# Kernel tuning notes

Hardware: AMD Instinct MI355X
Metric: run time of the kernel (lower is better)

The kernel has to match this reference:

```python
import jax, jax.numpy as jnp
import numpy as np


def _maxpool2x2(t):
    # t: [B, C, H, W] -> [B, C, H//2, W//2]
    b, c, h, w = t.shape
    return t.reshape(b, c, h // 2, 2, w // 2, 2).max(axis=(3, 5))


def setup_inputs() -> dict:
    key = jax.random.key(0)
    ks = jax.random.split(key, 6)
    B, C, H, W = 16, 64, 64, 64
    x = jax.random.normal(ks[0], (B, C, H, W), dtype=jnp.float32)
    # 1x1 conv weights (no bias), stored as [out_ch, in_ch]
    s = 0.05
    W_theta = jax.random.normal(ks[1], (C // 8, C), dtype=jnp.float32) * s
    W_phi = jax.random.normal(ks[2], (C // 8, C), dtype=jnp.float32) * s
    W_g = jax.random.normal(ks[3], (C // 2, C), dtype=jnp.float32) * s
    W_attn = jax.random.normal(ks[4], (C, C // 2), dtype=jnp.float32) * s
    sigma = jnp.ones((1,), dtype=jnp.float32) * 0.5  # nonzero so attn path matters
    return {"x": x, "W_theta": W_theta, "W_phi": W_phi, "W_g": W_g,
            "W_attn": W_attn, "sigma": sigma}


def reference(x, W_theta, W_phi, W_g, W_attn, sigma):
    B, C, H, W = x.shape
    N = H * W
    M = N // 4
    # 1x1 convs are channel matmuls
    theta = jnp.einsum('oc,bchw->bohw', W_theta, x).reshape(B, C // 8, N)      # [B, C/8, N]
    phi = _maxpool2x2(jnp.einsum('oc,bchw->bohw', W_phi, x)).reshape(B, C // 8, M)  # [B, C/8, M]
    attn = jax.nn.softmax(jnp.einsum('bkn,bkm->bnm', theta, phi), axis=-1)    # [B, N, M]
    g = _maxpool2x2(jnp.einsum('oc,bchw->bohw', W_g, x)).reshape(B, C // 2, M)  # [B, C/2, M]
    attn_g = jnp.einsum('bgm,bnm->bgn', g, attn).reshape(B, C // 2, H, W)      # [B, C/2, H, W]
    attn_g = jnp.einsum('oc,bchw->bohw', W_attn, attn_g)                        # [B, C, H, W]
    return x + sigma * attn_g
```

## Files before the change

### kernel.cpp

```cpp
#include <hip/hip_runtime.h>
#include <hip/hip_bf16.h>

#define CC 64
#define NN 4096
#define MM 1024

typedef __attribute__((ext_vector_type(4))) short s4b;
typedef __attribute__((ext_vector_type(8))) short s8b;
typedef __attribute__((ext_vector_type(4))) float float4v;

__device__ inline unsigned short f2bf(float f) {
    union { float f; unsigned u; } v; v.f = f;
    unsigned r = v.u + 0x7fff + ((v.u >> 16) & 1);
    return (unsigned short)(r >> 16);
}

__device__ inline float4v mfma16(s4b a, s4b b, float4v c) {
#if __has_builtin(__builtin_amdgcn_mfma_f32_16x16x16bf16_1k)
    return __builtin_amdgcn_mfma_f32_16x16x16bf16_1k(a, b, c, 0, 0, 0);
#else
    float4v d;
    asm volatile("v_mfma_f32_16x16x16_bf16 %0, %1, %2, %3"
                 : "=v"(d) : "v"(a), "v"(b), "v"(c));
    return d;
#endif
}

__device__ inline float4v mfma32(s8b a, s8b b, float4v c) {
#if __has_builtin(__builtin_amdgcn_mfma_f32_16x16x32_bf16)
    return __builtin_amdgcn_mfma_f32_16x16x32_bf16(a, b, c, 0, 0, 0);
#else
    float4v d;
    asm volatile("v_mfma_f32_16x16x32_bf16 %0, %1, %2, %3"
                 : "=v"(d) : "v"(a), "v"(b), "v"(c));
    return d;
#endif
}

__global__ __launch_bounds__(256) void prep_kernel(
    const float* __restrict__ x,
    const float* __restrict__ Wth,
    const float* __restrict__ Wph,
    const float* __restrict__ Wg,
    unsigned short* __restrict__ thT,
    unsigned short* __restrict__ phiP,
    unsigned short* __restrict__ gP)
{
    constexpr int XP = 72;
    constexpr int DP = 49;

    __shared__ __align__(16) union {
        unsigned short xs[128 * XP];
        float bufD[128 * DP];
    } sh;

    const int tid  = threadIdx.x;
    const int b    = blockIdx.y;
    const int hp   = blockIdx.x;
    const int lane = tid & 63;
    const int wv   = tid >> 6;
    const int c15  = lane & 15;
    const int quad = lane >> 4;
    const int n0row = hp * 128;

    s8b wf[3][2];
    {
        const float* base0 = (c15 < 8) ? (Wth + c15 * 64)
                                       : (Wph + (c15 - 8) * 64);
        const float* base1 = Wg + c15 * 64;
        const float* base2 = Wg + (16 + c15) * 64;
        const float* bases[3] = {base0, base1, base2};
#pragma unroll
        for (int t = 0; t < 3; ++t) {
#pragma unroll
            for (int s = 0; s < 2; ++s) {
                const float* p = bases[t] + s * 32 + quad * 8;
                const float4 w0 = *(const float4*)p;
                const float4 w1 = *(const float4*)(p + 4);
                union { unsigned short us[8]; s8b v; } tmp;
                tmp.us[0] = f2bf(w0.x); tmp.us[1] = f2bf(w0.y);
                tmp.us[2] = f2bf(w0.z); tmp.us[3] = f2bf(w0.w);
                tmp.us[4] = f2bf(w1.x); tmp.us[5] = f2bf(w1.y);
                tmp.us[6] = f2bf(w1.z); tmp.us[7] = f2bf(w1.w);
                wf[t][s] = tmp.v;
            }
        }
    }

    {
        const int spx = tid & 127;
        const int chp = tid >> 7;
        const float* xb = x + (size_t)b * CC * NN + n0row + spx;
#pragma unroll
        for (int i = 0; i < 16; ++i) {
            const int c0 = i * 4 + chp * 2;
            const float va = xb[(size_t)c0 * NN];
            const float vb = xb[(size_t)(c0 + 1) * NN];
            const unsigned pk = (unsigned)f2bf(va) |
                                ((unsigned)f2bf(vb) << 16);
            *(unsigned*)&sh.xs[spx * XP + c0] = pk;
        }
    }
    __syncthreads();

    float4v acc[2][3];
#pragma unroll
    for (int tl = 0; tl < 2; ++tl)
#pragma unroll
        for (int t = 0; t < 3; ++t)
            acc[tl][t] = float4v{0.f, 0.f, 0.f, 0.f};

#pragma unroll
    for (int tl = 0; tl < 2; ++tl) {
        const int p0 = wv * 32 + tl * 16;
#pragma unroll
        for (int s = 0; s < 2; ++s) {
            union { uint4 u; s8b v; } bx;
            bx.u = *(const uint4*)&sh.xs[(p0 + c15) * XP + s * 32 + quad * 8];
#pragma unroll
            for (int t = 0; t < 3; ++t)
                acc[tl][t] = mfma32(wf[t][s], bx.v, acc[tl][t]);
        }
    }
    __syncthreads();

#pragma unroll
    for (int tl = 0; tl < 2; ++tl) {
        const int p0 = wv * 32 + tl * 16;
#pragma unroll
        for (int t = 0; t < 3; ++t)
#pragma unroll
            for (int r = 0; r < 4; ++r)
                sh.bufD[(p0 + c15) * DP + t * 16 + quad * 4 + r]
                    = acc[tl][t][r];
    }
    __syncthreads();

    if (tid < 128) {
        const int px = tid;
        union { unsigned short s_[8]; uint4 v; } pk;
#pragma unroll
        for (int j = 0; j < 8; ++j)
            pk.s_[j] = f2bf(sh.bufD[px * DP + j] * 1.44269504f);
        *(uint4*)&thT[((size_t)b * NN + n0row + px) * 8] = pk.v;
    }

    for (int idx = tid; idx < 1280; idx += 256) {
        const int pm = idx & 31;
        const int jj = idx >> 5;
        const int p00 = 2 * pm, p10 = 64 + 2 * pm;
        const float v = fmaxf(
            fmaxf(sh.bufD[p00 * DP + 8 + jj], sh.bufD[(p00 + 1) * DP + 8 + jj]),
            fmaxf(sh.bufD[p10 * DP + 8 + jj], sh.bufD[(p10 + 1) * DP + 8 + jj]));
        const int m = hp * 32 + pm;
        if (jj < 8) phiP[((size_t)b * MM + m) * 8 + jj] = f2bf(v);
        else        gP[((size_t)b * 32 + (jj - 8)) * MM + m] = f2bf(v);
    }
}

__global__ __launch_bounds__(256) void attn_mfma(
    const unsigned short* __restrict__ thT,
    const unsigned short* __restrict__ phiP,
    const unsigned short* __restrict__ gP,
    const float* __restrict__ x,
    const float* __restrict__ Wa,
    const float* __restrict__ sigma,
    float* __restrict__ out)
{
    constexpr int GP = 264;
    constexpr int OBP = 40;

    __shared__ __align__(16) union {
        struct {
            unsigned short phi[256 * 8 + 16];
            unsigned short g[32 * GP];
        } m;
        struct {
            float part[18][128];
            unsigned short obb[64 * OBP];
        } cb;
    } sh;

    const int tid  = threadIdx.x;
    const int lane = tid & 63;
    const int wv   = tid >> 6;
    const int wq   = wv & 1;
    const int wk   = wv >> 1;
    const int c15  = lane & 15;
    const int quad = lane >> 4;
    const int b    = blockIdx.y;
    const int n0   = blockIdx.x * 64;

    union { unsigned short s[8]; s8b v; } wfrag;
    {
        const float* wr = Wa + (wv * 16 + c15) * 32 + quad * 8;
        const float4 w0 = *(const float4*)wr;
        const float4 w1 = *(const float4*)(wr + 4);
        wfrag.s[0] = f2bf(w0.x); wfrag.s[1] = f2bf(w0.y);
        wfrag.s[2] = f2bf(w0.z); wfrag.s[3] = f2bf(w0.w);
        wfrag.s[4] = f2bf(w1.x); wfrag.s[5] = f2bf(w1.y);
        wfrag.s[6] = f2bf(w1.z); wfrag.s[7] = f2bf(w1.w);
    }

    s4b zero4 = {0, 0, 0, 0};
    s4b bthA = zero4, bthB = zero4;
    if (quad < 2) {
        union { uint2 u; s4b s; } t;
        t.u = *(const uint2*)&thT[((size_t)b * NN + n0 + wq * 32 + c15) * 8 + quad * 4];
        bthA = t.s;
        t.u = *(const uint2*)&thT[((size_t)b * NN + n0 + wq * 32 + 16 + c15) * 8 + quad * 4];
        bthB = t.s;
    }

    float4v accA0 = {0.f, 0.f, 0.f, 0.f};
    float4v accA1 = {0.f, 0.f, 0.f, 0.f};
    float4v accB0 = {0.f, 0.f, 0.f, 0.f};
    float4v accB1 = {0.f, 0.f, 0.f, 0.f};
    float zaccA = 0.f, zaccB = 0.f;

    const int wk4 = wk * 4;

    const int sl_r  = tid & 7;
    const int sl_q3 = (tid >> 3) & 3;
    const int slot  = (tid & ~31) | ((sl_r >> 2) << 4) | (sl_q3 << 2) | (sl_r & 3);
    const size_t phi_base = ((size_t)b * MM + tid) * 8;
    size_t g_base[4];
    int    g_dst[4];
#pragma unroll
    for (int it = 0; it < 4; ++it) {
        const int idx  = tid + 256 * it;
        const int grow = idx >> 5, c32 = idx & 31;
        g_base[it] = ((size_t)b * 32 + grow) * MM + c32 * 8;
        g_dst[it]  = grow * GP + c32 * 8;
    }

    uint4 rphi = *(const uint4*)&phiP[phi_base];
    uint4 rg0  = *(const uint4*)&gP[g_base[0]];
    uint4 rg1  = *(const uint4*)&gP[g_base[1]];
    uint4 rg2  = *(const uint4*)&gP[g_base[2]];
    uint4 rg3  = *(const uint4*)&gP[g_base[3]];

    for (int ch = 0; ch < 4; ++ch) {
        __syncthreads();
        *(uint4*)&sh.m.phi[slot * 8] = rphi;
        if (tid < 2) {
            uint4 z4; z4.x = z4.y = z4.z = z4.w = 0u;
            *(uint4*)&sh.m.phi[256 * 8 + tid * 8] = z4;
        }
        *(uint4*)&sh.m.g[g_dst[0]] = rg0;
        *(uint4*)&sh.m.g[g_dst[1]] = rg1;
        *(uint4*)&sh.m.g[g_dst[2]] = rg2;
        *(uint4*)&sh.m.g[g_dst[3]] = rg3;
        if (ch < 3) {
            const size_t co = (size_t)(ch + 1) * 256;
            rphi = *(const uint4*)&phiP[phi_base + co * 8];
            rg0  = *(const uint4*)&gP[g_base[0] + co];
            rg1  = *(const uint4*)&gP[g_base[1] + co];
            rg2  = *(const uint4*)&gP[g_base[2] + co];
            rg3  = *(const uint4*)&gP[g_base[3] + co];
        }
        __syncthreads();

        const unsigned short* pA  = &sh.m.phi[c15 * 8 + quad * 4];
        const unsigned short* pg0 = &sh.m.g[c15 * GP + quad * 8];
        const unsigned short* pg1 = pg0 + 16 * GP;

#pragma unroll
        for (int s = 0; s < 4; ++s) {
            const int g32 = wk4 + s;

            union { uint2 u; s4b s_; } apA, apB;
            apA.u = *(const uint2*)&pA[g32 * 256];
            apB.u = *(const uint2*)&pA[g32 * 256 + 128];

            float4v cz = {0.f, 0.f, 0.f, 0.f};
            float4v sAlo = mfma16(apA.s_, bthA, cz);
            float4v sAhi = mfma16(apB.s_, bthA, cz);
            float4v sBlo = mfma16(apA.s_, bthB, cz);
            float4v sBhi = mfma16(apB.s_, bthB, cz);

            union { float f; unsigned u; } a0, a1, a2, a3, b0, b1, b2, b3;
            a0.f = __builtin_amdgcn_exp2f(sAlo[0]);
            a1.f = __builtin_amdgcn_exp2f(sAlo[1]);
            a2.f = __builtin_amdgcn_exp2f(sAlo[2]);
            a3.f = __builtin_amdgcn_exp2f(sAlo[3]);
            b0.f = __builtin_amdgcn_exp2f(sAhi[0]);
            b1.f = __builtin_amdgcn_exp2f(sAhi[1]);
            b2.f = __builtin_amdgcn_exp2f(sAhi[2]);
            b3.f = __builtin_amdgcn_exp2f(sAhi[3]);
            zaccA += ((a0.f + a1.f) + (a2.f + a3.f)) +
                     ((b0.f + b1.f) + (b2.f + b3.f));
            union { uint4 u; s8b s_; } paA;
            paA.u.x = __builtin_amdgcn_perm(a1.u, a0.u, 0x07060302u);
            paA.u.y = __builtin_amdgcn_perm(a3.u, a2.u, 0x07060302u);
            paA.u.z = __builtin_amdgcn_perm(b1.u, b0.u, 0x07060302u);
            paA.u.w = __builtin_amdgcn_perm(b3.u, b2.u, 0x07060302u);

            a0.f = __builtin_amdgcn_exp2f(sBlo[0]);
            a1.f = __builtin_amdgcn_exp2f(sBlo[1]);
            a2.f = __builtin_amdgcn_exp2f(sBlo[2]);
            a3.f = __builtin_amdgcn_exp2f(sBlo[3]);
            b0.f = __builtin_amdgcn_exp2f(sBhi[0]);
            b1.f = __builtin_amdgcn_exp2f(sBhi[1]);
            b2.f = __builtin_amdgcn_exp2f(sBhi[2]);
            b3.f = __builtin_amdgcn_exp2f(sBhi[3]);
            zaccB += ((a0.f + a1.f) + (a2.f + a3.f)) +
                     ((b0.f + b1.f) + (b2.f + b3.f));
            union { uint4 u; s8b s_; } paB;
            paB.u.x = __builtin_amdgcn_perm(a1.u, a0.u, 0x07060302u);
            paB.u.y = __builtin_amdgcn_perm(a3.u, a2.u, 0x07060302u);
            paB.u.z = __builtin_amdgcn_perm(b1.u, b0.u, 0x07060302u);
            paB.u.w = __builtin_amdgcn_perm(b3.u, b2.u, 0x07060302u);

            union { uint4 u; s8b s_; } bg0, bg1;
            bg0.u = *(const uint4*)&pg0[g32 * 32];
            bg1.u = *(const uint4*)&pg1[g32 * 32];

            accA0 = mfma32(paA.s_, bg0.s_, accA0);
            accA1 = mfma32(paA.s_, bg1.s_, accA1);
            accB0 = mfma32(paB.s_, bg0.s_, accB0);
            accB1 = mfma32(paB.s_, bg1.s_, accB1);
        }
    }

    __syncthreads();
    if (wk == 1) {
#pragma unroll
        for (int r = 0; r < 4; ++r) {
            sh.cb.part[     r][wq * 64 + lane] = accA0[r];
            sh.cb.part[ 4 + r][wq * 64 + lane] = accA1[r];
            sh.cb.part[ 8 + r][wq * 64 + lane] = accB0[r];
            sh.cb.part[12 + r][wq * 64 + lane] = accB1[r];
        }
        sh.cb.part[16][wq * 64 + lane] = zaccA;
        sh.cb.part[17][wq * 64 + lane] = zaccB;
    }
    __syncthreads();

    if (wk == 0) {
#pragma unroll
        for (int r = 0; r < 4; ++r) {
            accA0[r] += sh.cb.part[     r][wq * 64 + lane];
            accA1[r] += sh.cb.part[ 4 + r][wq * 64 + lane];
            accB0[r] += sh.cb.part[ 8 + r][wq * 64 + lane];
            accB1[r] += sh.cb.part[12 + r][wq * 64 + lane];
        }
        zaccA += sh.cb.part[16][wq * 64 + lane];
        zaccB += sh.cb.part[17][wq * 64 + lane];

        float zA = zaccA, zB = zaccB;
        zA += __shfl_xor(zA, 16, 64);
        zA += __shfl_xor(zA, 32, 64);
        zB += __shfl_xor(zB, 16, 64);
        zB += __shfl_xor(zB, 32, 64);
        const float rzqA = __builtin_amdgcn_rcpf(zA);
        const float rzqB = __builtin_amdgcn_rcpf(zB);

#pragma unroll
        for (int r = 0; r < 4; ++r) {
            const float rzA = __shfl(rzqA, quad * 4 + r, 64);
            const float rzB = __shfl(rzqB, quad * 4 + r, 64);
            const int qlA = wq * 32 + quad * 4 + r;
            const int qlB = qlA + 16;
            sh.cb.obb[qlA * OBP + c15]      = f2bf(accA0[r] * rzA);
            sh.cb.obb[qlA * OBP + 16 + c15] = f2bf(accA1[r] * rzA);
            sh.cb.obb[qlB * OBP + c15]      = f2bf(accB0[r] * rzB);
            sh.cb.obb[qlB * OBP + 16 + c15] = f2bf(accB1[r] * rzB);
        }
    }
    __syncthreads();

    const float sg = sigma[0];
#pragma unroll
    for (int t = 0; t < 4; ++t) {
        union { uint4 u; s8b s_; } bo;
        bo.u = *(const uint4*)&sh.cb.obb[(t * 16 + c15) * OBP + quad * 8];
        float4v cz = {0.f, 0.f, 0.f, 0.f};
        float4v oc = mfma32(wfrag.v, bo.s_, cz);
#pragma unroll
        for (int r = 0; r < 4; ++r) {
            const size_t oi = ((size_t)b * CC + wv * 16 + quad * 4 + r) * NN
                              + n0 + t * 16 + c15;
            const float xv_ = __builtin_nontemporal_load(&x[oi]);
            __builtin_nontemporal_store(xv_ + sg * oc[r], &out[oi]);
        }
    }
}

extern "C" void kernel_launch(void* const* d_in, const int* in_sizes, int n_in,
                              void* d_out, int out_size, void* d_ws, size_t ws_size,
                              hipStream_t stream) {
    const float* x      = (const float*)d_in[0];
    const float* W_th   = (const float*)d_in[1];
    const float* W_ph   = (const float*)d_in[2];
    const float* W_g    = (const float*)d_in[3];
    const float* W_attn = (const float*)d_in[4];
    const float* sigma  = (const float*)d_in[5];
    float* out = (float*)d_out;

    const int B = 16;
    unsigned short* thT  = (unsigned short*)d_ws;
    unsigned short* phiP = thT + (size_t)B * NN * 8;
    unsigned short* gP   = phiP + (size_t)B * MM * 8;

    prep_kernel<<<dim3(32, 16), 256, 0, stream>>>(x, W_th, W_ph, W_g,
                                                  thT, phiP, gP);
    attn_mfma<<<dim3(64, 16), 256, 0, stream>>>(thT, phiP, gP, x,
                                                W_attn, sigma, out);
}
```

Measured before the change: 97.92 us.

## Remap blocks per XCD and stage epilogue through LDS for wide coalesced stores

New measurement: 99.94 us. +2.1%, slower.

```diff
diff --git a/kernel.cpp b/kernel.cpp
--- a/kernel.cpp
+++ b/kernel.cpp
@@ -55,8 +55,11 @@
     } sh;
 
     const int tid  = threadIdx.x;
-    const int b    = blockIdx.y;
-    const int hp   = blockIdx.x;
+    const int bid  = blockIdx.x;
+    const int xcd  = bid & 7;
+    const int idx  = bid >> 3;
+    const int b    = xcd * 2 + (idx >> 5);
+    const int hp   = idx & 31;
     const int lane = tid & 63;
     const int wv   = tid >> 6;
     const int c15  = lane & 15;
@@ -145,9 +148,9 @@
         *(uint4*)&thT[((size_t)b * NN + n0row + px) * 8] = pk.v;
     }
 
-    for (int idx = tid; idx < 1280; idx += 256) {
-        const int pm = idx & 31;
-        const int jj = idx >> 5;
+    for (int idx2 = tid; idx2 < 1280; idx2 += 256) {
+        const int pm = idx2 & 31;
+        const int jj = idx2 >> 5;
         const int p00 = 2 * pm, p10 = 64 + 2 * pm;
         const float v = fmaxf(
             fmaxf(sh.bufD[p00 * DP + 8 + jj], sh.bufD[(p00 + 1) * DP + 8 + jj]),
@@ -167,8 +170,9 @@
     const float* __restrict__ sigma,
     float* __restrict__ out)
 {
-    constexpr int GP = 264;
+    constexpr int GP  = 264;
     constexpr int OBP = 40;
+    constexpr int OFP = 68;
 
     __shared__ __align__(16) union {
         struct {
@@ -178,6 +182,7 @@
         struct {
             float part[18][128];
             unsigned short obb[64 * OBP];
+            float obf[64][OFP];
         } cb;
     } sh;
 
@@ -188,8 +193,11 @@
     const int wk   = wv >> 1;
     const int c15  = lane & 15;
     const int quad = lane >> 4;
-    const int b    = blockIdx.y;
-    const int n0   = blockIdx.x * 64;
+    const int bid  = blockIdx.x;
+    const int xcd  = bid & 7;
+    const int idx  = bid >> 3;
+    const int b    = xcd * 2 + (idx >> 6);
+    const int n0   = (idx & 63) * 64;
 
     union { unsigned short s[8]; s8b v; } wfrag;
     {
@@ -228,8 +236,8 @@
     int    g_dst[4];
 #pragma unroll
     for (int it = 0; it < 4; ++it) {
-        const int idx  = tid + 256 * it;
-        const int grow = idx >> 5, c32 = idx & 31;
+        const int idx2 = tid + 256 * it;
+        const int grow = idx2 >> 5, c32 = idx2 & 31;
         g_base[it] = ((size_t)b * 32 + grow) * MM + c32 * 8;
         g_dst[it]  = grow * GP + c32 * 8;
     }
@@ -370,7 +378,6 @@
     }
     __syncthreads();
 
-    const float sg = sigma[0];
 #pragma unroll
     for (int t = 0; t < 4; ++t) {
         union { uint4 u; s8b s_; } bo;
@@ -378,12 +385,28 @@
         float4v cz = {0.f, 0.f, 0.f, 0.f};
         float4v oc = mfma32(wfrag.v, bo.s_, cz);
 #pragma unroll
-        for (int r = 0; r < 4; ++r) {
-            const size_t oi = ((size_t)b * CC + wv * 16 + quad * 4 + r) * NN
-                              + n0 + t * 16 + c15;
-            const float xv_ = __builtin_nontemporal_load(&x[oi]);
-            __builtin_nontemporal_store(xv_ + sg * oc[r], &out[oi]);
-        }
+        for (int r = 0; r < 4; ++r)
+            sh.cb.obf[wv * 16 + quad * 4 + r][t * 16 + c15] = oc[r];
+    }
+    __syncthreads();
+
+    const float sg = sigma[0];
+    const int orow = tid >> 4;
+    const int c4   = (tid & 15) * 4;
+#pragma unroll
+    for (int p = 0; p < 4; ++p) {
+        const int o = p * 16 + orow;
+        const float* of = &sh.cb.obf[o][c4];
+        const size_t oi = ((size_t)b * CC + o) * NN + n0 + c4;
+        float4 xv_;
+        xv_.x = __builtin_nontemporal_load(&x[oi]);
+        xv_.y = __builtin_nontemporal_load(&x[oi + 1]);
+        xv_.z = __builtin_nontemporal_load(&x[oi + 2]);
+        xv_.w = __builtin_nontemporal_load(&x[oi + 3]);
+        __builtin_nontemporal_store(xv_.x + sg * of[0], &out[oi]);
+        __builtin_nontemporal_store(xv_.y + sg * of[1], &out[oi + 1]);
+        __builtin_nontemporal_store(xv_.z + sg * of[2], &out[oi + 2]);
+        __builtin_nontemporal_store(xv_.w + sg * of[3], &out[oi + 3]);
     }
 }
 
@@ -403,8 +426,8 @@
     unsigned short* phiP = thT + (size_t)B * NN * 8;
     unsigned short* gP   = phiP + (size_t)B * MM * 8;
 
-    prep_kernel<<<dim3(32, 16), 256, 0, stream>>>(x, W_th, W_ph, W_g,
-                                                  thT, phiP, gP);
-    attn_mfma<<<dim3(64, 16), 256, 0, stream>>>(thT, phiP, gP, x,
-                                                W_attn, sigma, out);
-}
+    prep_kernel<<<dim3(512), 256, 0, stream>>>(x, W_th, W_ph, W_g,
+                                               thT, phiP, gP);
+    attn_mfma<<<dim3(1024), 256, 0, stream>>>(thT, phiP, gP, x,
+                                              W_attn, sigma, out);
+}
```
